# Performance work log

Measured on AMD Instinct MI355X. Metric: run time of the kernel, lower is better.

The kernel has to match this reference:

```python
import jax, jax.numpy as jnp
import numpy as np
import math

B, S, E = 8, 128, 192
H = 6
HD = E // H  # 32
L = 64       # latent_dim (hardcoded default in MHLA)
N_EXP = 8
TOP_K = 2
ED = 768     # expert_dim
EPS = 1e-5


def setup_inputs() -> dict:
    key = jax.random.key(0)
    ks = jax.random.split(key, 24)
    sc = 0.02
    nrm = lambda k, shp: (jax.random.normal(k, shp, dtype=jnp.float32) * sc)
    inp = {
        "x": jax.random.normal(ks[0], (B, S, E), dtype=jnp.float32),
        "rms1_w": jnp.ones((E,), jnp.float32),
        "rms2_w": jnp.ones((E,), jnp.float32),
        # latent_tokens: Linear(S*E -> L*E); stored [in, out]
        "latW": nrm(ks[1], (S * E, L * E)),
        "latb": jnp.zeros((L * E,), jnp.float32),
        "qW": nrm(ks[2], (E, E)), "qb": jnp.zeros((E,), jnp.float32),
        "kW": nrm(ks[3], (E, E)), "kb": jnp.zeros((E,), jnp.float32),
        "vW": nrm(ks[4], (E, E)), "vb": jnp.zeros((E,), jnp.float32),
        "oW": nrm(ks[5], (E, E)), "ob": jnp.zeros((E,), jnp.float32),
        "rW": nrm(ks[6], (E, N_EXP)), "rb": jnp.zeros((N_EXP,), jnp.float32),
        # stacked expert params: layer1 (E->ED), swiglu-linear (ED->ED), layer2 (ED->E)
        "e1W": nrm(ks[7], (N_EXP, E, ED)), "e1b": jnp.zeros((N_EXP, ED), jnp.float32),
        "swW": nrm(ks[8], (N_EXP, ED, ED)), "swb": jnp.zeros((N_EXP, ED), jnp.float32),
        "e2W": nrm(ks[9], (N_EXP, ED, E)), "e2b": jnp.zeros((N_EXP, E), jnp.float32),
    }
    return inp


def _rmsnorm(x, w):
    ms = jnp.mean(x * x, axis=-1, keepdims=True)
    return x * jax.lax.rsqrt(ms + EPS) * w


def _rope_q(q):
    # q: [B,H,S,HD]; rotate interleaved pairs, torch-style view(..., HD//2, 2)
    t = jnp.arange(S, dtype=jnp.float32)
    inv_freq = 1.0 / (10000.0 ** (jnp.arange(0, HD, 2, dtype=jnp.float32) / HD))
    freqs = jnp.outer(t, inv_freq)            # [S, HD/2]
    cos, sin = jnp.cos(freqs), jnp.sin(freqs)
    qp = q.reshape(B, H, S, HD // 2, 2)
    x1, x2 = qp[..., 0], qp[..., 1]
    r1 = x1 * cos - x2 * sin
    r2 = x1 * sin + x2 * cos
    return jnp.stack([r1, r2], axis=-1).reshape(B, H, S, HD)


def _mhla(x, latW, latb, qW, qb, kW, kb, vW, vb, oW, ob):
    latent = (x.reshape(B, S * E) @ latW + latb).reshape(B, L, E)
    q = (x @ qW + qb).reshape(B, S, H, HD).transpose(0, 2, 1, 3)       # [B,H,S,HD]
    k = (latent @ kW + kb).reshape(B, L, H, HD).transpose(0, 2, 1, 3)  # [B,H,L,HD]
    v = (latent @ vW + vb).reshape(B, L, H, HD).transpose(0, 2, 1, 3)
    qr = _rope_q(q)  # RoPE applied to query only (key_r = key in source)
    scores = jnp.einsum("bhsd,bhld->bhsl", qr, k) / math.sqrt(HD)
    attn = jax.nn.softmax(scores, axis=-1)
    out = jnp.einsum("bhsl,bhld->bhsd", attn, v)
    out = out.transpose(0, 2, 1, 3).reshape(B, S, E)
    return out @ oW + ob


def _moe(h, rW, rb, e1W, e1b, swW, swb, e2W, e2b):
    probs = jax.nn.softmax(h @ rW + rb, axis=-1)          # [B,S,N]
    pk, idx = jax.lax.top_k(probs, TOP_K)                 # [B,S,K]
    # dense all-expert compute (8 small experts), then gather top-k
    t1 = jnp.einsum("bse,neh->bsnh", h, e1W) + e1b        # [B,S,N,ED]
    t2 = jax.nn.relu(jnp.einsum("bsnh,nhg->bsng", t1, swW) + swb)
    eo = jnp.einsum("bsng,nge->bsne", t2, e2W) + e2b      # [B,S,N,E]
    sel = jnp.take_along_axis(eo, idx[..., None], axis=2) # [B,S,K,E]
    return jnp.sum(pk[..., None] * sel, axis=2)


def reference(x, rms1_w, rms2_w, latW, latb, qW, qb, kW, kb, vW, vb, oW, ob,
              rW, rb, e1W, e1b, swW, swb, e2W, e2b):
    x = x + _mhla(_rmsnorm(x, rms1_w), latW, latb, qW, qb, kW, kb, vW, vb, oW, ob)
    x = x + _moe(_rmsnorm(x, rms2_w), rW, rb, e1W, e1b, swW, swb, e2W, e2b)
    return x
```

## Files before the change

### kernel.cpp

```cpp
#include <hip/hip_runtime.h>
#include <hip/hip_bf16.h>
#include <math.h>

#define B 8
#define S 128
#define E 192
#define H 6
#define HD 32
#define L 64
#define NEXP 8
#define ED 768
#define T (B*S)
#define SE (S*E)
#define LE (L*E)

#define SPLITS 64
#define ISPAN 384
#define CHUNK 128

using s8 = __attribute__((ext_vector_type(8))) short;
using f4 = __attribute__((ext_vector_type(4))) float;

__global__ __launch_bounds__(64) void rmsnorm_k(const float* __restrict__ x,
                                                const float* __restrict__ w,
                                                float* __restrict__ y) {
  int row = blockIdx.x;
  int lane = threadIdx.x;
  const float* xr = x + (size_t)row * E;
  float v0 = xr[lane], v1 = xr[lane + 64], v2 = xr[lane + 128];
  float s = v0 * v0 + v1 * v1 + v2 * v2;
#pragma unroll
  for (int off = 32; off > 0; off >>= 1) s += __shfl_xor(s, off);
  float inv = rsqrtf(s * (1.0f / E) + 1e-5f);
  float* yr = y + (size_t)row * E;
  yr[lane]       = v0 * inv * w[lane];
  yr[lane + 64]  = v1 * inv * w[lane + 64];
  yr[lane + 128] = v2 * inv * w[lane + 128];
}

__global__ __launch_bounds__(64) void rmsnorm_bf_k(const float* __restrict__ x,
                                                   const float* __restrict__ w,
                                                   float* __restrict__ y,
                                                   __hip_bfloat16* __restrict__ yb) {
  int row = blockIdx.x;
  int lane = threadIdx.x;
  const float* xr = x + (size_t)row * E;
  float v0 = xr[lane], v1 = xr[lane + 64], v2 = xr[lane + 128];
  float s = v0 * v0 + v1 * v1 + v2 * v2;
#pragma unroll
  for (int off = 32; off > 0; off >>= 1) s += __shfl_xor(s, off);
  float inv = rsqrtf(s * (1.0f / E) + 1e-5f);
  float r0 = v0 * inv * w[lane];
  float r1 = v1 * inv * w[lane + 64];
  float r2 = v2 * inv * w[lane + 128];
  float* yr = y + (size_t)row * E;
  __hip_bfloat16* yrb = yb + (size_t)row * E;
  yr[lane] = r0; yr[lane + 64] = r1; yr[lane + 128] = r2;
  yrb[lane] = __float2bfloat16(r0);
  yrb[lane + 64] = __float2bfloat16(r1);
  yrb[lane + 128] = __float2bfloat16(r2);
}

__global__ __launch_bounds__(256) void lat_partial_k(const float* __restrict__ xn,
                                                     const float* __restrict__ latW,
                                                     float* __restrict__ part) {
  const int tid = threadIdx.x;
  const int j = blockIdx.x * 1024 + tid * 4;
  const int i0 = blockIdx.y * ISPAN;
  __shared__ float xs[CHUNK][8];
  f4 acc[8];
#pragma unroll
  for (int b = 0; b < 8; ++b) acc[b] = (f4){0.f, 0.f, 0.f, 0.f};
  for (int c = 0; c < ISPAN; c += CHUNK) {
    float* xsf = (float*)xs;
    __syncthreads();
    for (int l = tid; l < CHUNK * 8; l += 256) {
      int ii = l >> 3, b = l & 7;
      xsf[l] = xn[(size_t)b * SE + i0 + c + ii];
    }
    __syncthreads();
#pragma unroll 8
    for (int ii = 0; ii < CHUNK; ++ii) {
      const f4 w = __builtin_nontemporal_load(
          (const f4*)&latW[(size_t)(i0 + c + ii) * LE + j]);
#pragma unroll
      for (int b = 0; b < 8; ++b) {
        float xv = xs[ii][b];
        acc[b][0] += xv * w[0];
        acc[b][1] += xv * w[1];
        acc[b][2] += xv * w[2];
        acc[b][3] += xv * w[3];
      }
    }
  }
#pragma unroll
  for (int b = 0; b < 8; ++b)
    *(f4*)&part[((size_t)blockIdx.y * 8 + b) * LE + j] = acc[b];
}

__global__ __launch_bounds__(256) void lat_reduce_k(const float* __restrict__ part,
                                                    const float* __restrict__ latb,
                                                    float* __restrict__ lat) {
  int g = blockIdx.x * 256 + threadIdx.x;
  int b = g / LE, j = g - b * LE;
  float s = latb[j];
  for (int sp = 0; sp < SPLITS; ++sp) s += part[((size_t)sp * 8 + b) * LE + j];
  lat[g] = s;
}

__global__ __launch_bounds__(256) void qkv_k(const float* __restrict__ xn,
                                             const float* __restrict__ lat,
                                             const float* __restrict__ qW, const float* __restrict__ qb,
                                             const float* __restrict__ kW, const float* __restrict__ kb,
                                             const float* __restrict__ vW, const float* __restrict__ vb,
                                             float* __restrict__ qo,
                                             float* __restrict__ ko,
                                             float* __restrict__ vo) {
  const int z = blockIdx.z;
  const float* A = (z == 0) ? xn : lat;
  const float* W = (z == 0) ? qW : (z == 1) ? kW : vW;
  const float* bp = (z == 0) ? qb : (z == 1) ? kb : vb;
  float* C = (z == 0) ? qo : (z == 1) ? ko : vo;
  const int M = (z == 0) ? T : (B * L);
  const int m0 = blockIdx.y * 64;
  if (m0 >= M) return;
  const int n0 = blockIdx.x * 64;
  __shared__ float As[16][64];
  __shared__ float Ws[16][64];
  const int tid = threadIdx.x;
  const int tx = tid & 15, ty = tid >> 4;
  const int arow = tid >> 2, acol = (tid & 3) << 2;
  const int wrow = tid >> 4, wcol = (tid & 15) << 2;
  float acc[4][4] = {{0.f}};
  for (int kb2 = 0; kb2 < E; kb2 += 16) {
    float4 a = *(const float4*)&A[(size_t)(m0 + arow) * E + kb2 + acol];
    As[acol][arow] = a.x;
    As[acol + 1][arow] = a.y;
    As[acol + 2][arow] = a.z;
    As[acol + 3][arow] = a.w;
    *(float4*)&Ws[wrow][wcol] = *(const float4*)&W[(size_t)(kb2 + wrow) * E + n0 + wcol];
    __syncthreads();
#pragma unroll
    for (int k = 0; k < 16; ++k) {
      float4 a4 = *(const float4*)&As[k][ty << 2];
      float4 w4 = *(const float4*)&Ws[k][tx << 2];
      acc[0][0] += a4.x * w4.x; acc[0][1] += a4.x * w4.y; acc[0][2] += a4.x * w4.z; acc[0][3] += a4.x * w4.w;
      acc[1][0] += a4.y * w4.x; acc[1][1] += a4.y * w4.y; acc[1][2] += a4.y * w4.z; acc[1][3] += a4.y * w4.w;
      acc[2][0] += a4.z * w4.x; acc[2][1] += a4.z * w4.y; acc[2][2] += a4.z * w4.z; acc[2][3] += a4.z * w4.w;
      acc[3][0] += a4.w * w4.x; acc[3][1] += a4.w * w4.y; acc[3][2] += a4.w * w4.z; acc[3][3] += a4.w * w4.w;
    }
    __syncthreads();
  }
#pragma unroll
  for (int i = 0; i < 4; ++i) {
    int m = m0 + (ty << 2) + i;
#pragma unroll
    for (int jj = 0; jj < 4; ++jj) {
      int n = n0 + (tx << 2) + jj;
      C[(size_t)m * E + n] = acc[i][jj] + bp[n];
    }
  }
}

__global__ __launch_bounds__(256) void gemm_k(const float* __restrict__ A,
                                              const float* __restrict__ W,
                                              const float* __restrict__ bias,
                                              const float* __restrict__ resid,
                                              float* __restrict__ C,
                                              int M, int N, int K,
                                              int flags) {
  const int n0 = blockIdx.x * 64;
  const int m0 = blockIdx.y * 64;
  __shared__ float As[16][64];
  __shared__ float Ws[16][64];
  const int tid = threadIdx.x;
  const int tx = tid & 15, ty = tid >> 4;
  const int arow = tid >> 2, acol = (tid & 3) << 2;
  const int wrow = tid >> 4, wcol = (tid & 15) << 2;
  float acc[4][4] = {{0.f}};
  for (int kb = 0; kb < K; kb += 16) {
    float4 a = *(const float4*)&A[(size_t)(m0 + arow) * K + kb + acol];
    As[acol][arow] = a.x;
    As[acol + 1][arow] = a.y;
    As[acol + 2][arow] = a.z;
    As[acol + 3][arow] = a.w;
    *(float4*)&Ws[wrow][wcol] = *(const float4*)&W[(size_t)(kb + wrow) * N + n0 + wcol];
    __syncthreads();
#pragma unroll
    for (int k = 0; k < 16; ++k) {
      float4 a4 = *(const float4*)&As[k][ty << 2];
      float4 w4 = *(const float4*)&Ws[k][tx << 2];
      acc[0][0] += a4.x * w4.x; acc[0][1] += a4.x * w4.y; acc[0][2] += a4.x * w4.z; acc[0][3] += a4.x * w4.w;
      acc[1][0] += a4.y * w4.x; acc[1][1] += a4.y * w4.y; acc[1][2] += a4.y * w4.z; acc[1][3] += a4.y * w4.w;
      acc[2][0] += a4.z * w4.x; acc[2][1] += a4.z * w4.y; acc[2][2] += a4.z * w4.z; acc[2][3] += a4.z * w4.w;
      acc[3][0] += a4.w * w4.x; acc[3][1] += a4.w * w4.y; acc[3][2] += a4.w * w4.z; acc[3][3] += a4.w * w4.w;
    }
    __syncthreads();
  }
#pragma unroll
  for (int i = 0; i < 4; ++i) {
    int m = m0 + (ty << 2) + i;
#pragma unroll
    for (int j = 0; j < 4; ++j) {
      int n = n0 + (tx << 2) + j;
      float v = acc[i][j];
      if (bias) v += bias[n];
      if (flags & 1) v = fmaxf(v, 0.f);
      if (flags & 2) v += resid[(size_t)m * N + n];
      C[(size_t)m * N + n] = v;
    }
  }
}

__global__ __launch_bounds__(256) void tconv_k(const float* __restrict__ in,
                                               __hip_bfloat16* __restrict__ out,
                                               int K, int N) {
  const int e = blockIdx.z;
  in += (size_t)e * K * N;
  out += (size_t)e * N * K;
  __shared__ float tile[32][33];
  int tx = threadIdx.x & 31, r8 = threadIdx.x >> 5;
  int k0 = blockIdx.x * 32, n0 = blockIdx.y * 32;
#pragma unroll
  for (int i = 0; i < 4; ++i)
    tile[r8 + 8 * i][tx] = in[(size_t)(k0 + r8 + 8 * i) * N + n0 + tx];
  __syncthreads();
#pragma unroll
  for (int i = 0; i < 4; ++i) {
    int nr = r8 + 8 * i;
    out[(size_t)(n0 + nr) * K + k0 + tx] = __float2bfloat16(tile[tx][nr]);
  }
}

__global__ __launch_bounds__(256) void moe_gemm_k(const __hip_bfloat16* __restrict__ A_,
                                                  const __hip_bfloat16* __restrict__ Wt_,
                                                  const float* __restrict__ bias_,
                                                  void* __restrict__ C_,
                                                  int M, int N, int K,
                                                  long aB, long wB, long bB, long cB,
                                                  int flags) {
  const int e = blockIdx.z;
  const short* A = (const short*)A_ + (size_t)e * aB;
  const short* Wt = (const short*)Wt_ + (size_t)e * wB;
  const float* bias = bias_ + (size_t)e * bB;
  const int n0 = blockIdx.x * 64;
  const int m0 = blockIdx.y * 128;
  __shared__ short As[128 * 64];
  __shared__ short Bs[64 * 64];
  const int tid = threadIdx.x;
  const int lane = tid & 63, wid = tid >> 6;
  const int wr = wid >> 1, wc = wid & 1;
  const int lr = lane & 15, lg = lane >> 4;
  f4 acc[4][2];
#pragma unroll
  for (int fm = 0; fm < 4; ++fm)
#pragma unroll
    for (int fn = 0; fn < 2; ++fn) acc[fm][fn] = (f4){0.f, 0.f, 0.f, 0.f};

  for (int kb = 0; kb < K; kb += 64) {
    __syncthreads();
#pragma unroll
    for (int p = 0; p < 4; ++p) {
      int eidx = p * 256 + tid;
      int row = eidx >> 3, slot = eidx & 7;
      s8 v = *(const s8*)(A + (size_t)(m0 + row) * K + kb + slot * 8);
      *(s8*)&As[row * 64 + ((slot ^ (row & 7)) << 3)] = v;
    }
#pragma unroll
    for (int p = 0; p < 2; ++p) {
      int eidx = p * 256 + tid;
      int row = eidx >> 3, slot = eidx & 7;
      s8 v = *(const s8*)(Wt + (size_t)(n0 + row) * K + kb + slot * 8);
      *(s8*)&Bs[row * 64 + ((slot ^ (row & 7)) << 3)] = v;
    }
    __syncthreads();
#pragma unroll
    for (int kk = 0; kk < 64; kk += 32) {
      const int sb = (kk >> 3) + lg;
      s8 af[4], bf[2];
#pragma unroll
      for (int fm = 0; fm < 4; ++fm) {
        int row = wr * 64 + fm * 16 + lr;
        af[fm] = *(const s8*)&As[row * 64 + ((sb ^ (row & 7)) << 3)];
      }
#pragma unroll
      for (int fn = 0; fn < 2; ++fn) {
        int row = wc * 32 + fn * 16 + lr;
        bf[fn] = *(const s8*)&Bs[row * 64 + ((sb ^ (row & 7)) << 3)];
      }
#pragma unroll
      for (int fm = 0; fm < 4; ++fm)
#pragma unroll
        for (int fn = 0; fn < 2; ++fn)
          acc[fm][fn] = __builtin_amdgcn_mfma_f32_16x16x32_bf16(af[fm], bf[fn], acc[fm][fn], 0, 0, 0);
    }
  }
#pragma unroll
  for (int fm = 0; fm < 4; ++fm) {
#pragma unroll
    for (int fn = 0; fn < 2; ++fn) {
      int col = n0 + wc * 32 + fn * 16 + lr;
      int rowb = m0 + wr * 64 + fm * 16 + lg * 4;
      float bv = bias[col];
#pragma unroll
      for (int j = 0; j < 4; ++j) {
        float v = acc[fm][fn][j] + bv;
        if (flags & 1) v = fmaxf(v, 0.f);
        if (flags & 2)
          ((float*)C_)[(size_t)e * cB + (size_t)(rowb + j) * N + col] = v;
        else
          ((__hip_bfloat16*)C_)[(size_t)e * cB + (size_t)(rowb + j) * N + col] = __float2bfloat16(v);
      }
    }
  }
}

__global__ __launch_bounds__(128) void attn_k(const float* __restrict__ q,
                                              const float* __restrict__ kk,
                                              const float* __restrict__ vv,
                                              float* __restrict__ ao) {
  int b = blockIdx.x / H, h = blockIdx.x % H;
  __shared__ float ks[64][32], vs[64][32];
  int tid = threadIdx.x;
  {
    int l = tid >> 1, hf = (tid & 1) * 16;
    const float4* ksrc = (const float4*)&kk[(size_t)(b * L + l) * E + h * HD + hf];
    const float4* vsrc = (const float4*)&vv[(size_t)(b * L + l) * E + h * HD + hf];
    float4* kdst = (float4*)&ks[l][hf];
    float4* vdst = (float4*)&vs[l][hf];
#pragma unroll
    for (int u = 0; u < 4; ++u) { kdst[u] = ksrc[u]; vdst[u] = vsrc[u]; }
  }
  __syncthreads();
  int s = tid;
  const float* qp = &q[(size_t)(b * S + s) * E + h * HD];
  float qv[32];
#pragma unroll
  for (int d = 0; d < 32; ++d) qv[d] = qp[d];
#pragma unroll
  for (int d = 0; d < 16; ++d) {
    float invf = exp2f(-(float)d * (13.287712379549449f / 16.0f));
    float ang = (float)s * invf;
    float sn, cs;
    __sincosf(ang, &sn, &cs);
    float x1 = qv[2 * d], x2 = qv[2 * d + 1];
    qv[2 * d] = x1 * cs - x2 * sn;
    qv[2 * d + 1] = x1 * sn + x2 * cs;
  }
  const float scale = 0.17677669529663687f;
  float mx = -1e30f;
  for (int l = 0; l < 64; ++l) {
    float dot = 0.f;
#pragma unroll
    for (int d = 0; d < 32; ++d) dot += qv[d] * ks[l][d];
    mx = fmaxf(mx, dot * scale);
  }
  float o[32];
#pragma unroll
  for (int d = 0; d < 32; ++d) o[d] = 0.f;
  float sum = 0.f;
  for (int l = 0; l < 64; ++l) {
    float dot = 0.f;
#pragma unroll
    for (int d = 0; d < 32; ++d) dot += qv[d] * ks[l][d];
    float wgt = __expf(dot * scale - mx);
    sum += wgt;
#pragma unroll
    for (int d = 0; d < 32; ++d) o[d] += wgt * vs[l][d];
  }
  float inv = 1.0f / sum;
  float* op = &ao[(size_t)(b * S + s) * E + h * HD];
#pragma unroll
  for (int d = 0; d < 32; ++d) op[d] = o[d] * inv;
}

__global__ __launch_bounds__(64) void router_k(const float* __restrict__ hbuf,
                                               const float* __restrict__ rW,
                                               const float* __restrict__ rb,
                                               float* __restrict__ pk,
                                               int* __restrict__ idx) {
  int t = blockIdx.x * 64 + threadIdx.x;
  float lg[8];
#pragma unroll
  for (int n = 0; n < 8; ++n) lg[n] = rb[n];
  const float* hp = &hbuf[(size_t)t * E];
  for (int e2 = 0; e2 < E; ++e2) {
    float hv = hp[e2];
    const float* wr = &rW[e2 * 8];
#pragma unroll
    for (int n = 0; n < 8; ++n) lg[n] += hv * wr[n];
  }
  float mx = lg[0];
#pragma unroll
  for (int n = 1; n < 8; ++n) mx = fmaxf(mx, lg[n]);
  float p[8], sum = 0.f;
#pragma unroll
  for (int n = 0; n < 8; ++n) { p[n] = __expf(lg[n] - mx); sum += p[n]; }
  float inv = 1.f / sum;
#pragma unroll
  for (int n = 0; n < 8; ++n) p[n] *= inv;
  int i0 = 0;
#pragma unroll
  for (int n = 1; n < 8; ++n) if (p[n] > p[i0]) i0 = n;
  int i1 = (i0 == 0) ? 1 : 0;
#pragma unroll
  for (int n = 0; n < 8; ++n) if (n != i0 && p[n] > p[i1]) i1 = n;
  pk[t * 2] = p[i0];
  pk[t * 2 + 1] = p[i1];
  idx[t * 2] = i0;
  idx[t * 2 + 1] = i1;
}

__global__ __launch_bounds__(256) void combine_k(const float* __restrict__ x1,
                                                 const float* __restrict__ eo,
                                                 const float* __restrict__ pk,
                                                 const int* __restrict__ idx,
                                                 float* __restrict__ out) {
  int g = blockIdx.x * 256 + threadIdx.x;
  int t = g / E;
  int e = g - t * E;
  int i0 = idx[t * 2], i1 = idx[t * 2 + 1];
  out[g] = x1[g] + pk[t * 2] * eo[((size_t)i0 * T + t) * E + e]
                 + pk[t * 2 + 1] * eo[((size_t)i1 * T + t) * E + e];
}

extern "C" void kernel_launch(void* const* d_in, const int* in_sizes, int n_in,
                              void* d_out, int out_size, void* d_ws, size_t ws_size,
                              hipStream_t stream) {
  const float* x    = (const float*)d_in[0];
  const float* r1w  = (const float*)d_in[1];
  const float* r2w  = (const float*)d_in[2];
  const float* latW = (const float*)d_in[3];
  const float* latb = (const float*)d_in[4];
  const float* qW   = (const float*)d_in[5];
  const float* qb   = (const float*)d_in[6];
  const float* kW   = (const float*)d_in[7];
  const float* kb   = (const float*)d_in[8];
  const float* vW   = (const float*)d_in[9];
  const float* vb   = (const float*)d_in[10];
  const float* oW   = (const float*)d_in[11];
  const float* ob   = (const float*)d_in[12];
  const float* rW   = (const float*)d_in[13];
  const float* rb   = (const float*)d_in[14];
  const float* e1W  = (const float*)d_in[15];
  const float* e1b  = (const float*)d_in[16];
  const float* swW  = (const float*)d_in[17];
  const float* swb  = (const float*)d_in[18];
  const float* e2W  = (const float*)d_in[19];
  const float* e2b  = (const float*)d_in[20];
  float* out = (float*)d_out;

  float* ws = (float*)d_ws;
  float* xn1  = ws;
  float* lat  = ws + 196608;
  float* qbuf = ws + 294912;
  float* kbuf = ws + 491520;
  float* vbuf = ws + 589824;
  float* ao   = ws + 688128;
  float* x1   = ws + 884736;
  float* hbuf = ws + 1081344;
  float* pk   = ws + 1277952;
  int*   idx  = (int*)(ws + 1280000);
  __hip_bfloat16* hb    = (__hip_bfloat16*)(ws + 1282048);
  __hip_bfloat16* e1Wt  = (__hip_bfloat16*)(ws + 1380352);
  __hip_bfloat16* swWt  = (__hip_bfloat16*)(ws + 1970176);
  __hip_bfloat16* e2Wt  = (__hip_bfloat16*)(ws + 4329472);
  __hip_bfloat16* t1    = (__hip_bfloat16*)(ws + 4919296);
  __hip_bfloat16* t2    = (__hip_bfloat16*)(ws + 8065024);
  float* eo   = ws + 11210752;
  float* part = ws + 12783616;

  tconv_k<<<dim3(E / 32, ED / 32, NEXP), 256, 0, stream>>>(e1W, e1Wt, E, ED);
  tconv_k<<<dim3(ED / 32, ED / 32, NEXP), 256, 0, stream>>>(swW, swWt, ED, ED);
  tconv_k<<<dim3(ED / 32, E / 32, NEXP), 256, 0, stream>>>(e2W, e2Wt, ED, E);

  rmsnorm_k<<<T, 64, 0, stream>>>(x, r1w, xn1);
  lat_partial_k<<<dim3(12, SPLITS), 256, 0, stream>>>(xn1, latW, part);
  lat_reduce_k<<<(8 * LE) / 256, 256, 0, stream>>>(part, latb, lat);
  qkv_k<<<dim3(3, 16, 3), 256, 0, stream>>>(xn1, lat, qW, qb, kW, kb, vW, vb,
                                            qbuf, kbuf, vbuf);
  attn_k<<<B * H, 128, 0, stream>>>(qbuf, kbuf, vbuf, ao);
  gemm_k<<<dim3(3, 16), 256, 0, stream>>>(ao, oW, ob, x, x1, T, E, E, 2);
  rmsnorm_bf_k<<<T, 64, 0, stream>>>(x1, r2w, hbuf, hb);
  router_k<<<T / 64, 64, 0, stream>>>(hbuf, rW, rb, pk, idx);
  moe_gemm_k<<<dim3(ED / 64, T / 128, NEXP), 256, 0, stream>>>(
      hb, e1Wt, e1b, t1, T, ED, E, 0, (long)ED * E, ED, (long)T * ED, 0);
  moe_gemm_k<<<dim3(ED / 64, T / 128, NEXP), 256, 0, stream>>>(
      t1, swWt, swb, t2, T, ED, ED, (long)T * ED, (long)ED * ED, ED, (long)T * ED, 1);
  moe_gemm_k<<<dim3(E / 64, T / 128, NEXP), 256, 0, stream>>>(
      t2, e2Wt, e2b, eo, T, E, ED, (long)T * ED, (long)E * ED, E, (long)T * E, 2);
  combine_k<<<(T * E) / 256, 256, 0, stream>>>(x1, eo, pk, idx, out);
}
```

Baseline: 348.6 us.

## Route tokens sparsely to experts with compacted token lists instead of dense MoE

Replaces the dense all-expert MoE compute with a gather-based grouped GEMM. A compaction kernel builds per-expert token lists from the top-2 router indices, and each expert GEMM only processes its assigned rows, with early exit for empty tiles. Combine reads outputs via the recorded positions. RMSNorm and the router are fused into one kernel, which drops the fp32 hbuf round-trip. Expected expert work drops to roughly a quarter, at the cost of a serial single-block compaction and possibly unbalanced tiles when routing is skewed.

Measured after the change: 340.4 us. -2.4%, faster.

```diff
diff --git a/kernel.cpp b/kernel.cpp
--- a/kernel.cpp
+++ b/kernel.cpp
@@ -36,29 +36,6 @@
   yr[lane]       = v0 * inv * w[lane];
   yr[lane + 64]  = v1 * inv * w[lane + 64];
   yr[lane + 128] = v2 * inv * w[lane + 128];
-}
-
-__global__ __launch_bounds__(64) void rmsnorm_bf_k(const float* __restrict__ x,
-                                                   const float* __restrict__ w,
-                                                   float* __restrict__ y,
-                                                   __hip_bfloat16* __restrict__ yb) {
-  int row = blockIdx.x;
-  int lane = threadIdx.x;
-  const float* xr = x + (size_t)row * E;
-  float v0 = xr[lane], v1 = xr[lane + 64], v2 = xr[lane + 128];
-  float s = v0 * v0 + v1 * v1 + v2 * v2;
-#pragma unroll
-  for (int off = 32; off > 0; off >>= 1) s += __shfl_xor(s, off);
-  float inv = rsqrtf(s * (1.0f / E) + 1e-5f);
-  float r0 = v0 * inv * w[lane];
-  float r1 = v1 * inv * w[lane + 64];
-  float r2 = v2 * inv * w[lane + 128];
-  float* yr = y + (size_t)row * E;
-  __hip_bfloat16* yrb = yb + (size_t)row * E;
-  yr[lane] = r0; yr[lane + 64] = r1; yr[lane + 128] = r2;
-  yrb[lane] = __float2bfloat16(r0);
-  yrb[lane + 64] = __float2bfloat16(r1);
-  yrb[lane + 128] = __float2bfloat16(r2);
 }
 
 __global__ __launch_bounds__(256) void lat_partial_k(const float* __restrict__ xn,
@@ -232,44 +209,135 @@
   }
 }
 
-__global__ __launch_bounds__(256) void moe_gemm_k(const __hip_bfloat16* __restrict__ A_,
+__global__ __launch_bounds__(64) void router_rms_k(const float* __restrict__ x1,
+                                                   const float* __restrict__ w,
+                                                   const float* __restrict__ rW,
+                                                   const float* __restrict__ rb,
+                                                   __hip_bfloat16* __restrict__ hb,
+                                                   float* __restrict__ pk,
+                                                   int* __restrict__ idx) {
+  int t = blockIdx.x;
+  int lane = threadIdx.x;
+  const float* xr = x1 + (size_t)t * E;
+  float v0 = xr[lane], v1 = xr[lane + 64], v2 = xr[lane + 128];
+  float s = v0 * v0 + v1 * v1 + v2 * v2;
+#pragma unroll
+  for (int off = 32; off > 0; off >>= 1) s += __shfl_xor(s, off);
+  float inv = rsqrtf(s * (1.0f / E) + 1e-5f);
+  float r0 = v0 * inv * w[lane];
+  float r1 = v1 * inv * w[lane + 64];
+  float r2 = v2 * inv * w[lane + 128];
+  __hip_bfloat16* yrb = hb + (size_t)t * E;
+  yrb[lane] = __float2bfloat16(r0);
+  yrb[lane + 64] = __float2bfloat16(r1);
+  yrb[lane + 128] = __float2bfloat16(r2);
+  float lg[8];
+#pragma unroll
+  for (int n = 0; n < 8; ++n)
+    lg[n] = r0 * rW[lane * 8 + n] + r1 * rW[(lane + 64) * 8 + n] + r2 * rW[(lane + 128) * 8 + n];
+#pragma unroll
+  for (int n = 0; n < 8; ++n)
+#pragma unroll
+    for (int off = 32; off > 0; off >>= 1) lg[n] += __shfl_xor(lg[n], off);
+  if (lane == 0) {
+#pragma unroll
+    for (int n = 0; n < 8; ++n) lg[n] += rb[n];
+    float mx = lg[0];
+#pragma unroll
+    for (int n = 1; n < 8; ++n) mx = fmaxf(mx, lg[n]);
+    float p[8], sum = 0.f;
+#pragma unroll
+    for (int n = 0; n < 8; ++n) { p[n] = __expf(lg[n] - mx); sum += p[n]; }
+    float isum = 1.f / sum;
+#pragma unroll
+    for (int n = 0; n < 8; ++n) p[n] *= isum;
+    int i0 = 0;
+#pragma unroll
+    for (int n = 1; n < 8; ++n) if (p[n] > p[i0]) i0 = n;
+    int i1 = (i0 == 0) ? 1 : 0;
+#pragma unroll
+    for (int n = 0; n < 8; ++n) if (n != i0 && p[n] > p[i1]) i1 = n;
+    pk[t * 2] = p[i0];
+    pk[t * 2 + 1] = p[i1];
+    idx[t * 2] = i0;
+    idx[t * 2 + 1] = i1;
+  }
+}
+
+__global__ __launch_bounds__(512) void compact_k(const int* __restrict__ idx,
+                                                 int* __restrict__ toklist,
+                                                 int* __restrict__ ppos,
+                                                 int* __restrict__ cnt) {
+  int e = threadIdx.x >> 6;
+  int lane = threadIdx.x & 63;
+  int pos = 0;
+  for (int base = 0; base < T; base += 64) {
+    int t = base + lane;
+    int i0 = idx[t * 2], i1 = idx[t * 2 + 1];
+    bool sel = (i0 == e) || (i1 == e);
+    unsigned long long m = __ballot(sel);
+    int myoff = __popcll(m & ((1ull << lane) - 1ull));
+    if (sel) {
+      int p = pos + myoff;
+      toklist[e * T + p] = t;
+      ppos[t * 2 + ((i0 == e) ? 0 : 1)] = p;
+    }
+    pos += __popcll(m);
+  }
+  if (lane == 0) cnt[e] = pos;
+}
+
+__global__ __launch_bounds__(256) void moe_gemm_g(const __hip_bfloat16* __restrict__ A_,
                                                   const __hip_bfloat16* __restrict__ Wt_,
                                                   const float* __restrict__ bias_,
                                                   void* __restrict__ C_,
-                                                  int M, int N, int K,
+                                                  const int* __restrict__ toklist,
+                                                  const int* __restrict__ cntp,
+                                                  int N, int K,
                                                   long aB, long wB, long bB, long cB,
                                                   int flags) {
   const int e = blockIdx.z;
-  const short* A = (const short*)A_ + (size_t)e * aB;
+  const int cnt = cntp[e];
+  const int m0 = blockIdx.y * 128;
+  if (m0 >= cnt) return;
+  const short* A = (const short*)A_ + ((flags & 4) ? 0 : (size_t)e * aB);
   const short* Wt = (const short*)Wt_ + (size_t)e * wB;
   const float* bias = bias_ + (size_t)e * bB;
   const int n0 = blockIdx.x * 64;
-  const int m0 = blockIdx.y * 128;
   __shared__ short As[128 * 64];
   __shared__ short Bs[64 * 64];
   const int tid = threadIdx.x;
   const int lane = tid & 63, wid = tid >> 6;
   const int wr = wid >> 1, wc = wid & 1;
   const int lr = lane & 15, lg = lane >> 4;
+  long arow_off[4];
+#pragma unroll
+  for (int p = 0; p < 4; ++p) {
+    int row = p * 32 + (tid >> 3);
+    int gr = m0 + row;
+    int src;
+    if (flags & 4) src = (gr < cnt) ? toklist[e * T + gr] : toklist[e * T];
+    else src = gr;
+    arow_off[p] = (size_t)src * K;
+  }
   f4 acc[4][2];
 #pragma unroll
   for (int fm = 0; fm < 4; ++fm)
 #pragma unroll
     for (int fn = 0; fn < 2; ++fn) acc[fm][fn] = (f4){0.f, 0.f, 0.f, 0.f};
 
+  const int slot = tid & 7;
   for (int kb = 0; kb < K; kb += 64) {
     __syncthreads();
 #pragma unroll
     for (int p = 0; p < 4; ++p) {
-      int eidx = p * 256 + tid;
-      int row = eidx >> 3, slot = eidx & 7;
-      s8 v = *(const s8*)(A + (size_t)(m0 + row) * K + kb + slot * 8);
+      int row = p * 32 + (tid >> 3);
+      s8 v = *(const s8*)(A + arow_off[p] + kb + slot * 8);
       *(s8*)&As[row * 64 + ((slot ^ (row & 7)) << 3)] = v;
     }
 #pragma unroll
     for (int p = 0; p < 2; ++p) {
-      int eidx = p * 256 + tid;
-      int row = eidx >> 3, slot = eidx & 7;
+      int row = p * 32 + (tid >> 3);
       s8 v = *(const s8*)(Wt + (size_t)(n0 + row) * K + kb + slot * 8);
       *(s8*)&Bs[row * 64 + ((slot ^ (row & 7)) << 3)] = v;
     }
@@ -304,6 +372,7 @@
       float bv = bias[col];
 #pragma unroll
       for (int j = 0; j < 4; ++j) {
+        if (rowb + j >= cnt) continue;
         float v = acc[fm][fn][j] + bv;
         if (flags & 1) v = fmaxf(v, 0.f);
         if (flags & 2)
@@ -374,54 +443,19 @@
   for (int d = 0; d < 32; ++d) op[d] = o[d] * inv;
 }
 
-__global__ __launch_bounds__(64) void router_k(const float* __restrict__ hbuf,
-                                               const float* __restrict__ rW,
-                                               const float* __restrict__ rb,
-                                               float* __restrict__ pk,
-                                               int* __restrict__ idx) {
-  int t = blockIdx.x * 64 + threadIdx.x;
-  float lg[8];
-#pragma unroll
-  for (int n = 0; n < 8; ++n) lg[n] = rb[n];
-  const float* hp = &hbuf[(size_t)t * E];
-  for (int e2 = 0; e2 < E; ++e2) {
-    float hv = hp[e2];
-    const float* wr = &rW[e2 * 8];
-#pragma unroll
-    for (int n = 0; n < 8; ++n) lg[n] += hv * wr[n];
-  }
-  float mx = lg[0];
-#pragma unroll
-  for (int n = 1; n < 8; ++n) mx = fmaxf(mx, lg[n]);
-  float p[8], sum = 0.f;
-#pragma unroll
-  for (int n = 0; n < 8; ++n) { p[n] = __expf(lg[n] - mx); sum += p[n]; }
-  float inv = 1.f / sum;
-#pragma unroll
-  for (int n = 0; n < 8; ++n) p[n] *= inv;
-  int i0 = 0;
-#pragma unroll
-  for (int n = 1; n < 8; ++n) if (p[n] > p[i0]) i0 = n;
-  int i1 = (i0 == 0) ? 1 : 0;
-#pragma unroll
-  for (int n = 0; n < 8; ++n) if (n != i0 && p[n] > p[i1]) i1 = n;
-  pk[t * 2] = p[i0];
-  pk[t * 2 + 1] = p[i1];
-  idx[t * 2] = i0;
-  idx[t * 2 + 1] = i1;
-}
-
 __global__ __launch_bounds__(256) void combine_k(const float* __restrict__ x1,
-                                                 const float* __restrict__ eo,
+                                                 const float* __restrict__ eoc,
                                                  const float* __restrict__ pk,
                                                  const int* __restrict__ idx,
+                                                 const int* __restrict__ ppos,
                                                  float* __restrict__ out) {
   int g = blockIdx.x * 256 + threadIdx.x;
   int t = g / E;
   int e = g - t * E;
   int i0 = idx[t * 2], i1 = idx[t * 2 + 1];
-  out[g] = x1[g] + pk[t * 2] * eo[((size_t)i0 * T + t) * E + e]
-                 + pk[t * 2 + 1] * eo[((size_t)i1 * T + t) * E + e];
+  int p0 = ppos[t * 2], p1 = ppos[t * 2 + 1];
+  out[g] = x1[g] + pk[t * 2] * eoc[((size_t)i0 * T + p0) * E + e]
+                 + pk[t * 2 + 1] * eoc[((size_t)i1 * T + p1) * E + e];
 }
 
 extern "C" void kernel_launch(void* const* d_in, const int* in_sizes, int n_in,
@@ -458,17 +492,19 @@
   float* vbuf = ws + 589824;
   float* ao   = ws + 688128;
   float* x1   = ws + 884736;
-  float* hbuf = ws + 1081344;
   float* pk   = ws + 1277952;
   int*   idx  = (int*)(ws + 1280000);
-  __hip_bfloat16* hb    = (__hip_bfloat16*)(ws + 1282048);
-  __hip_bfloat16* e1Wt  = (__hip_bfloat16*)(ws + 1380352);
-  __hip_bfloat16* swWt  = (__hip_bfloat16*)(ws + 1970176);
-  __hip_bfloat16* e2Wt  = (__hip_bfloat16*)(ws + 4329472);
-  __hip_bfloat16* t1    = (__hip_bfloat16*)(ws + 4919296);
-  __hip_bfloat16* t2    = (__hip_bfloat16*)(ws + 8065024);
-  float* eo   = ws + 11210752;
-  float* part = ws + 12783616;
+  int*   toklist = (int*)(ws + 1282048);
+  int*   ppos    = (int*)(ws + 1290240);
+  int*   cnt     = (int*)(ws + 1292288);
+  __hip_bfloat16* hb    = (__hip_bfloat16*)(ws + 1294336);
+  __hip_bfloat16* e1Wt  = (__hip_bfloat16*)(ws + 1392640);
+  __hip_bfloat16* swWt  = (__hip_bfloat16*)(ws + 1982464);
+  __hip_bfloat16* e2Wt  = (__hip_bfloat16*)(ws + 4341760);
+  __hip_bfloat16* t1    = (__hip_bfloat16*)(ws + 4931584);
+  __hip_bfloat16* t2    = (__hip_bfloat16*)(ws + 8077312);
+  float* eoc  = ws + 11223040;
+  float* part = ws + 12795904;
 
   tconv_k<<<dim3(E / 32, ED / 32, NEXP), 256, 0, stream>>>(e1W, e1Wt, E, ED);
   tconv_k<<<dim3(ED / 32, ED / 32, NEXP), 256, 0, stream>>>(swW, swWt, ED, ED);
@@ -481,13 +517,13 @@
                                             qbuf, kbuf, vbuf);
   attn_k<<<B * H, 128, 0, stream>>>(qbuf, kbuf, vbuf, ao);
   gemm_k<<<dim3(3, 16), 256, 0, stream>>>(ao, oW, ob, x, x1, T, E, E, 2);
-  rmsnorm_bf_k<<<T, 64, 0, stream>>>(x1, r2w, hbuf, hb);
-  router_k<<<T / 64, 64, 0, stream>>>(hbuf, rW, rb, pk, idx);
-  moe_gemm_k<<<dim3(ED / 64, T / 128, NEXP), 256, 0, stream>>>(
-      hb, e1Wt, e1b, t1, T, ED, E, 0, (long)ED * E, ED, (long)T * ED, 0);
-  moe_gemm_k<<<dim3(ED / 64, T / 128, NEXP), 256, 0, stream>>>(
-      t1, swWt, swb, t2, T, ED, ED, (long)T * ED, (long)ED * ED, ED, (long)T * ED, 1);
-  moe_gemm_k<<<dim3(E / 64, T / 128, NEXP), 256, 0, stream>>>(
-      t2, e2Wt, e2b, eo, T, E, ED, (long)T * ED, (long)E * ED, E, (long)T * E, 2);
-  combine_k<<<(T * E) / 256, 256, 0, stream>>>(x1, eo, pk, idx, out);
-}
+  router_rms_k<<<T, 64, 0, stream>>>(x1, r2w, rW, rb, hb, pk, idx);
+  compact_k<<<1, 512, 0, stream>>>(idx, toklist, ppos, cnt);
+  moe_gemm_g<<<dim3(ED / 64, 8, NEXP), 256, 0, stream>>>(
+      hb, e1Wt, e1b, t1, toklist, cnt, ED, E, 0, (long)ED * E, ED, (long)T * ED, 4);
+  moe_gemm_g<<<dim3(ED / 64, 8, NEXP), 256, 0, stream>>>(
+      t1, swWt, swb, t2, toklist, cnt, ED, ED, (long)T * ED, (long)ED * ED, ED, (long)T * ED, 1);
+  moe_gemm_g<<<dim3(E / 64, 8, NEXP), 256, 0, stream>>>(
+      t2, e2Wt, e2b, eoc, toklist, cnt, E, ED, (long)T * ED, (long)E * ED, E, (long)T * E, 2);
+  combine_k<<<(T * E) / 256, 256, 0, stream>>>(x1, eoc, pk, idx, ppos, out);
+}
```
